# Performance work log

Measured on AMD Instinct MI355X. Metric: run time of the kernel, lower is better.

Reference implementation:

```python
import jax, jax.numpy as jnp
import numpy as np

B, S, V, E, H, L = 32, 512, 32000, 256, 512, 48


def setup_inputs() -> dict:
    key = jax.random.key(0)
    ks = jax.random.split(key, 12)
    tokens = jax.random.randint(ks[0], (B, S), 0, V)
    length = jax.random.randint(ks[1], (B,), S // 2, S + 1)
    labels = jax.random.randint(ks[2], (B, S), 0, L)
    embed_table = jax.random.normal(ks[3], (V, E), jnp.float32) * 0.1
    embed_table = embed_table.at[0].set(0.0)  # padding_idx = 0
    # torch LSTM gate order: i, f, g, o ; b = b_ih + b_hh folded together
    w_ih_f = jax.random.normal(ks[4], (4 * H, E), jnp.float32) * 0.05
    w_hh_f = jax.random.normal(ks[5], (4 * H, H), jnp.float32) * 0.05
    b_f = jnp.zeros((4 * H,), jnp.float32)
    w_ih_b = jax.random.normal(ks[6], (4 * H, E), jnp.float32) * 0.05
    w_hh_b = jax.random.normal(ks[7], (4 * H, H), jnp.float32) * 0.05
    b_b = jnp.zeros((4 * H,), jnp.float32)
    w_em = jax.random.normal(ks[8], (L, 2 * H), jnp.float32) * 0.02
    b_em = jnp.zeros((L,), jnp.float32)
    transition = jax.random.uniform(ks[9], (L, L), jnp.float32)  # torch.rand init
    return {"tokens": tokens, "length": length, "labels": labels,
            "embed_table": embed_table,
            "w_ih_f": w_ih_f, "w_hh_f": w_hh_f, "b_f": b_f,
            "w_ih_b": w_ih_b, "w_hh_b": w_hh_b, "b_b": b_b,
            "w_em": w_em, "b_em": b_em, "transition": transition}


def _lstm_dir(x, w_ih, w_hh, b, reverse):
    # x: [B,S,E] -> hidden states [B,S,H]
    xw = jnp.einsum('bse,ge->bsg', x, w_ih) + b  # precompute input projection [B,S,4H]
    if reverse:
        xw = xw[:, ::-1]
    Bn = x.shape[0]
    Hn = w_hh.shape[1]
    h0 = jnp.zeros((Bn, Hn), x.dtype)
    c0 = jnp.zeros((Bn, Hn), x.dtype)

    def step(carry, xt):
        h, c = carry
        gates = xt + h @ w_hh.T  # [B,4H]
        i, f, g, o = jnp.split(gates, 4, axis=-1)
        i = jax.nn.sigmoid(i)
        f = jax.nn.sigmoid(f)
        g = jnp.tanh(g)
        o = jax.nn.sigmoid(o)
        c = f * c + i * g
        h = o * jnp.tanh(c)
        return (h, c), h

    _, hs = jax.lax.scan(step, (h0, c0), jnp.swapaxes(xw, 0, 1))
    hs = jnp.swapaxes(hs, 0, 1)  # [B,S,H]
    if reverse:
        hs = hs[:, ::-1]
    return hs


def reference(tokens, length, labels, embed_table,
              w_ih_f, w_hh_f, b_f, w_ih_b, w_hh_b, b_b,
              w_em, b_em, transition):
    x = embed_table[tokens]                      # [B,S,E]
    hf = _lstm_dir(x, w_ih_f, w_hh_f, b_f, reverse=False)
    hb = _lstm_dir(x, w_ih_b, w_hh_b, b_b, reverse=True)
    h = jnp.concatenate([hf, hb], axis=-1)       # [B,S,2H]
    logits = jnp.einsum('bsh,lh->bsl', h, w_em) + b_em
    e = jnp.exp(logits)                          # emission = exp(linear), as in source
    T = jnp.exp(transition)                      # transition = exp(param), as in source
    Bn, Sn = tokens.shape
    pos = jnp.arange(Sn)[None, :]
    mask = pos < length[:, None]                 # [B,S] valid positions

    # gold path score: sum emissions over valid steps + transitions between them
    em_real = jnp.take_along_axis(e, labels[..., None], axis=-1)[..., 0]  # [B,S]
    real = jnp.sum(em_real * mask, axis=-1)
    trans_real = T[labels[:, :-1], labels[:, 1:]]                          # [B,S-1]
    real = real + jnp.sum(trans_real * mask[:, 1:], axis=-1)

    # forward algorithm, exactly as written in source:
    # alpha_new[k] = logsumexp_l( alpha[k] + T[k,l] + e_t[l] )
    alpha0 = e[:, 0, :]                          # [B,L]

    def step(alpha, inp):
        et, mt = inp                             # [B,L], [B]
        scores = alpha[:, :, None] + T[None, :, :] + et[:, None, :]  # [B,L,L]
        new = jax.nn.logsumexp(scores, axis=-1)
        alpha = jnp.where(mt[:, None], new, alpha)
        return alpha, None

    alpha, _ = jax.lax.scan(step, alpha0,
                            (jnp.swapaxes(e[:, 1:], 0, 1),
                             jnp.swapaxes(mask[:, 1:], 0, 1)))
    sum_score = jax.nn.logsumexp(alpha, axis=-1)  # [B]
    return sum_score - real                       # negative log probability per example
```

## Files before the change

### kernel.cpp

```cpp
#include <hip/hip_runtime.h>
#include <math.h>
#include <stdint.h>

#define Bn 32
#define Sn 512
#define En 256
#define Hn 512
#define Ln 48
#define G4 2048
#define NWG 32

typedef unsigned short u16;
typedef __attribute__((ext_vector_type(8))) __bf16 bf16x8;
typedef __attribute__((ext_vector_type(4))) float f32x4;

__device__ inline float bf2f(u16 u) {
    return __uint_as_float(((unsigned)u) << 16);
}
__device__ inline u16 f2bf(float f) {
    unsigned u = __float_as_uint(f);
    unsigned r = (u + 0x7fffu + ((u >> 16) & 1u)) >> 16;
    return (u16)r;
}
__device__ inline float sigmoidf_(float x) { return 1.f / (1.f + expf(-x)); }
__device__ inline float tanh_fast(float x) { return 2.f / (1.f + expf(-2.f * x)) - 1.f; }

__global__ __launch_bounds__(256) void prep_kernel(
    const int* __restrict__ tokens, const float* __restrict__ embed,
    const float* __restrict__ wihf, const float* __restrict__ wihb,
    const float* __restrict__ whhf, const float* __restrict__ whhb,
    const float* __restrict__ wem, const float* __restrict__ trans,
    u16* __restrict__ xbf, u16* __restrict__ wihf_b, u16* __restrict__ wihb_b,
    u16* __restrict__ whhf_b, u16* __restrict__ whhb_b, u16* __restrict__ wem_b,
    float* __restrict__ expT, float* __restrict__ alphaAcc,
    float* __restrict__ realAcc, unsigned* __restrict__ flags)
{
    size_t idx = (size_t)blockIdx.x * blockDim.x + threadIdx.x;
    size_t stride = (size_t)gridDim.x * blockDim.x;
    for (size_t i = idx; i < (size_t)Bn * Sn * En; i += stride) {
        size_t n = i >> 8; int ee = (int)(i & 255);
        int tok = tokens[n];
        xbf[i] = f2bf(embed[(size_t)tok * En + ee]);
    }
    for (size_t i = idx; i < (size_t)G4 * En; i += stride) {
        wihf_b[i] = f2bf(wihf[i]); wihb_b[i] = f2bf(wihb[i]);
    }
    for (size_t i = idx; i < (size_t)G4 * Hn; i += stride) {
        whhf_b[i] = f2bf(whhf[i]); whhb_b[i] = f2bf(whhb[i]);
    }
    for (size_t i = idx; i < (size_t)Ln * 2 * Hn; i += stride) wem_b[i] = f2bf(wem[i]);
    for (size_t i = idx; i < (size_t)Ln * Ln; i += stride) expT[i] = expf(trans[i]);
    for (size_t i = idx; i < (size_t)Bn * Ln; i += stride) alphaAcc[i] = 0.f;
    for (size_t i = idx; i < (size_t)Bn; i += stride) realAcc[i] = 0.f;
    for (size_t i = idx; i < (size_t)2 * Sn * NWG; i += stride) flags[i] = 0u;
}

__global__ __launch_bounds__(256) void gemm_xw(
    const u16* __restrict__ xbf, const u16* __restrict__ wihf_b,
    const u16* __restrict__ wihb_b, const float* __restrict__ bias_f,
    const float* __restrict__ bias_b, u16* __restrict__ xw_f, u16* __restrict__ xw_b)
{
    int mb = blockIdx.x, nb = blockIdx.y, dir = blockIdx.z;
    const u16* wih = dir ? wihb_b : wihf_b;
    const float* bias = dir ? bias_b : bias_f;
    u16* xw = dir ? xw_b : xw_f;

    __shared__ u16 At[64 * 136];
    __shared__ u16 Bt[64 * 136];

    int tid = threadIdx.x;
    int w = tid >> 6, lane = tid & 63;
    int lm = lane & 15, lkq = (lane >> 4) * 8;
    int Moff = (w & 1) * 32, Noff = (w >> 1) * 32;

    f32x4 zero = {0.f, 0.f, 0.f, 0.f};
    f32x4 acc[2][2] = {{zero, zero}, {zero, zero}};

    for (int kc = 0; kc < 2; kc++) {
        for (int c = tid; c < 1024; c += 256) {
            int r = c >> 4, cc = (c & 15) * 8;
            *(bf16x8*)&At[r * 136 + cc] =
                *(const bf16x8*)&xbf[((size_t)(mb * 64 + r)) * En + kc * 128 + cc];
            *(bf16x8*)&Bt[r * 136 + cc] =
                *(const bf16x8*)&wih[((size_t)(nb * 64 + r)) * En + kc * 128 + cc];
        }
        __syncthreads();
        #pragma unroll
        for (int ks = 0; ks < 4; ks++) {
            int k = ks * 32 + lkq;
            bf16x8 a0 = *(const bf16x8*)&At[(Moff + lm) * 136 + k];
            bf16x8 a1 = *(const bf16x8*)&At[(Moff + 16 + lm) * 136 + k];
            bf16x8 b0 = *(const bf16x8*)&Bt[(Noff + lm) * 136 + k];
            bf16x8 b1 = *(const bf16x8*)&Bt[(Noff + 16 + lm) * 136 + k];
            acc[0][0] = __builtin_amdgcn_mfma_f32_16x16x32_bf16(a0, b0, acc[0][0], 0, 0, 0);
            acc[0][1] = __builtin_amdgcn_mfma_f32_16x16x32_bf16(a0, b1, acc[0][1], 0, 0, 0);
            acc[1][0] = __builtin_amdgcn_mfma_f32_16x16x32_bf16(a1, b0, acc[1][0], 0, 0, 0);
            acc[1][1] = __builtin_amdgcn_mfma_f32_16x16x32_bf16(a1, b1, acc[1][1], 0, 0, 0);
        }
        __syncthreads();
    }
    #pragma unroll
    for (int mi = 0; mi < 2; mi++)
        #pragma unroll
        for (int ni = 0; ni < 2; ni++)
            #pragma unroll
            for (int reg = 0; reg < 4; reg++) {
                int row = Moff + mi * 16 + (lane >> 4) * 4 + reg;
                int col = Noff + ni * 16 + lm;
                int n = mb * 64 + row;
                int g = nb * 64 + col;
                int t = n & 511, b = n >> 9;
                float v = acc[mi][ni][reg] + bias[g];
                xw[((size_t)t * Bn + b) * G4 + g] = f2bf(v);
            }
}

__global__ __launch_bounds__(512) void lstm_rec(
    const u16* __restrict__ whhf_b, const u16* __restrict__ whhb_b,
    const u16* __restrict__ xw_f, const u16* __restrict__ xw_b,
    u16* __restrict__ hf, u16* __restrict__ hb, unsigned* __restrict__ flags)
{
    int wg = blockIdx.x;
    int dir = wg >> 5;
    int w = wg & 31;
    const u16* __restrict__ whh = dir ? whhb_b : whhf_b;
    const u16* __restrict__ xw  = dir ? xw_b  : xw_f;
    u16* __restrict__ hbuf = dir ? hb : hf;
    unsigned* flg = flags + (size_t)dir * Sn * NWG;

    __shared__ u16 Hs[32 * 512];
    __shared__ float Cp[4 * 32 * 17];
    __shared__ u16 hout[32 * 16];

    int tid = threadIdx.x;
    int wv = tid >> 6, lane = tid & 63;
    int lm = lane & 15, kq = lane >> 4;
    int mt = wv & 1, nt = wv >> 1;
    int b = tid >> 4, hc = tid & 15;

    bf16x8 Bf[16];
    {
        const u16* wrow = &whh[((size_t)nt * Hn + (size_t)w * 16 + lm) * Hn];
        #pragma unroll
        for (int ks = 0; ks < 16; ks++)
            Bf[ks] = *(const bf16x8*)&wrow[ks * 32 + kq * 8];
    }

    float c_state = 0.f;
    const f32x4 zero = {0.f, 0.f, 0.f, 0.f};

    for (int it = 0; it < Sn; it++) {
        int t = dir ? (Sn - 1 - it) : it;
        f32x4 acc = zero;

        if (it > 0) {
            int tprev = dir ? (t + 1) : (t - 1);
            if (tid < 64) {
                const unsigned* fp = flg + (size_t)(it - 1) * NWG + (tid & 31);
                int tries = 0;
                while (true) {
                    unsigned v;
                    asm volatile("global_load_dword %0, %1, off sc0 sc1\n\t"
                                 "s_waitcnt vmcnt(0)"
                                 : "=v"(v) : "v"(fp) : "memory");
                    if (__all(v != 0) || ++tries > 10000) break;
                    __builtin_amdgcn_s_sleep(1);
                }
            }
            __syncthreads();
            {
                const u16* base = &hbuf[((size_t)b * Sn + tprev) * Hn];
                const u16* p0 = base + (hc + 0) * 8;
                const u16* p1 = base + (hc + 16) * 8;
                const u16* p2 = base + (hc + 32) * 8;
                const u16* p3 = base + (hc + 48) * 8;
                f32x4 h0, h1, h2, h3;
                asm volatile(
                    "global_load_dwordx4 %0, %4, off sc0 sc1\n\t"
                    "global_load_dwordx4 %1, %5, off sc0 sc1\n\t"
                    "global_load_dwordx4 %2, %6, off sc0 sc1\n\t"
                    "global_load_dwordx4 %3, %7, off sc0 sc1\n\t"
                    "s_waitcnt vmcnt(0)"
                    : "=v"(h0), "=v"(h1), "=v"(h2), "=v"(h3)
                    : "v"(p0), "v"(p1), "v"(p2), "v"(p3)
                    : "memory");
                *(f32x4*)&Hs[(b * 64 + ((hc + 0) ^ (b & 7))) * 8] = h0;
                *(f32x4*)&Hs[(b * 64 + ((hc + 16) ^ (b & 7))) * 8] = h1;
                *(f32x4*)&Hs[(b * 64 + ((hc + 32) ^ (b & 7))) * 8] = h2;
                *(f32x4*)&Hs[(b * 64 + ((hc + 48) ^ (b & 7))) * 8] = h3;
            }
            __syncthreads();
            #pragma unroll
            for (int ks = 0; ks < 16; ks++) {
                bf16x8 a = *(const bf16x8*)
                    &Hs[((mt * 16 + lm) * 64 + ((ks * 4 + kq) ^ (lm & 7))) * 8];
                acc = __builtin_amdgcn_mfma_f32_16x16x32_bf16(a, Bf[ks], acc, 0, 0, 0);
            }
        }

        const u16* xp = &xw[((size_t)t * Bn + b) * G4 + (size_t)w * 16 + hc];
        float xg0 = bf2f(xp[0 * Hn]);
        float xg1 = bf2f(xp[1 * Hn]);
        float xg2 = bf2f(xp[2 * Hn]);
        float xg3 = bf2f(xp[3 * Hn]);

        #pragma unroll
        for (int reg = 0; reg < 4; reg++)
            Cp[(nt * 32 + mt * 16 + kq * 4 + reg) * 17 + lm] = acc[reg];
        __syncthreads();

        float g0 = Cp[(0 * 32 + b) * 17 + hc] + xg0;
        float g1 = Cp[(1 * 32 + b) * 17 + hc] + xg1;
        float g2 = Cp[(2 * 32 + b) * 17 + hc] + xg2;
        float g3 = Cp[(3 * 32 + b) * 17 + hc] + xg3;
        float i_ = sigmoidf_(g0);
        float f_ = sigmoidf_(g1);
        float gg = tanh_fast(g2);
        float o_ = sigmoidf_(g3);
        c_state = f_ * c_state + i_ * gg;
        float hv = o_ * tanh_fast(c_state);
        hout[tid] = f2bf(hv);
        __syncthreads();

        if (tid < 64) {
            int bq = lane >> 1, half = lane & 1;
            f32x4 hv8 = *(const f32x4*)&hout[lane * 8];
            u16* sp = &hbuf[((size_t)bq * Sn + t) * Hn + (size_t)w * 16 + half * 8];
            asm volatile("global_store_dwordx4 %0, %1, off sc0 sc1"
                         :: "v"(sp), "v"(hv8) : "memory");
            asm volatile("s_waitcnt vmcnt(0)" ::: "memory");
            if (tid == 0) {
                unsigned one = 1;
                unsigned* fq = flg + (size_t)it * NWG + w;
                asm volatile("global_store_dword %0, %1, off sc0 sc1\n\t"
                             "s_waitcnt vmcnt(0)"
                             :: "v"(fq), "v"(one) : "memory");
            }
        }
    }
}

__global__ __launch_bounds__(256) void emis(
    const u16* __restrict__ hf, const u16* __restrict__ hb,
    const u16* __restrict__ wem_b, const float* __restrict__ bem,
    float* __restrict__ e)
{
    int mb = blockIdx.x;
    int tid = threadIdx.x, wv = tid >> 6, lane = tid & 63;
    int lm = lane & 15, lkq = (lane >> 4) * 8;
    int row = mb * 64 + wv * 16;

    f32x4 zero = {0.f, 0.f, 0.f, 0.f};
    f32x4 acc[3] = {zero, zero, zero};
    for (int ks = 0; ks < 32; ks++) {
        int k = ks * 32 + lkq;
        const u16* hsrc = (ks < 16) ? &hf[(size_t)(row + lm) * Hn + k]
                                    : &hb[(size_t)(row + lm) * Hn + (k - 512)];
        bf16x8 a = *(const bf16x8*)hsrc;
        #pragma unroll
        for (int nt = 0; nt < 3; nt++) {
            bf16x8 bfr = *(const bf16x8*)&wem_b[(size_t)(nt * 16 + lm) * 1024 + k];
            acc[nt] = __builtin_amdgcn_mfma_f32_16x16x32_bf16(a, bfr, acc[nt], 0, 0, 0);
        }
    }
    #pragma unroll
    for (int nt = 0; nt < 3; nt++)
        #pragma unroll
        for (int reg = 0; reg < 4; reg++) {
            int r = row + (lane >> 4) * 4 + reg;
            int col = nt * 16 + lm;
            float lg = acc[nt][reg] + bem[col];
            e[(size_t)r * Ln + col] = expf(lg);
        }
}

__global__ __launch_bounds__(64) void crf_step(
    const float* __restrict__ e, const float* __restrict__ expT,
    const int* __restrict__ labels, const int* __restrict__ lengths,
    float* __restrict__ alphaAcc, float* __restrict__ realAcc)
{
    int bt = blockIdx.x;
    int b = bt >> 9, t = bt & 511;
    __shared__ float er[Ln];
    int tid = threadIdx.x;
    if (tid < Ln) er[tid] = e[(size_t)bt * Ln + tid];
    __syncthreads();
    bool inlen = t < lengths[b];
    if (t >= 1 && inlen && tid < Ln) {
        int i = tid;
        float m = -1e30f;
        for (int j = 0; j < Ln; j++) m = fmaxf(m, expT[i * Ln + j] + er[j]);
        float s = 0.f;
        for (int j = 0; j < Ln; j++) s += expf(expT[i * Ln + j] + er[j] - m);
        atomicAdd(&alphaAcc[b * Ln + i], m + logf(s));
    }
    if (tid == 0 && inlen) {
        int lab = labels[b * Sn + t];
        float r = er[lab];
        if (t >= 1) r += expT[labels[b * Sn + t - 1] * Ln + lab];
        atomicAdd(&realAcc[b], r);
    }
}

__global__ __launch_bounds__(64) void finalize(
    const float* __restrict__ e, const float* __restrict__ alphaAcc,
    const float* __restrict__ realAcc, float* __restrict__ out)
{
    int b = threadIdx.x;
    if (b >= Bn) return;
    float m = -1e30f;
    for (int i = 0; i < Ln; i++) {
        float a = e[((size_t)b * Sn) * Ln + i] + alphaAcc[b * Ln + i];
        m = fmaxf(m, a);
    }
    float s = 0.f;
    for (int i = 0; i < Ln; i++) {
        float a = e[((size_t)b * Sn) * Ln + i] + alphaAcc[b * Ln + i];
        s += expf(a - m);
    }
    out[b] = m + logf(s) - realAcc[b];
}

extern "C" void kernel_launch(void* const* d_in, const int* in_sizes, int n_in,
                              void* d_out, int out_size, void* d_ws, size_t ws_size,
                              hipStream_t stream)
{
    const int*   tokens = (const int*)d_in[0];
    const int*   length = (const int*)d_in[1];
    const int*   labels = (const int*)d_in[2];
    const float* embed  = (const float*)d_in[3];
    const float* wihf   = (const float*)d_in[4];
    const float* whhf   = (const float*)d_in[5];
    const float* bf     = (const float*)d_in[6];
    const float* wihb   = (const float*)d_in[7];
    const float* whhb   = (const float*)d_in[8];
    const float* bbv    = (const float*)d_in[9];
    const float* wem    = (const float*)d_in[10];
    const float* bem    = (const float*)d_in[11];
    const float* trans  = (const float*)d_in[12];
    float* out = (float*)d_out;

    char* p = (char*)d_ws;
    auto take = [&](size_t bytes) -> char* {
        char* q = p;
        p += (bytes + 255) & ~(size_t)255;
        return q;
    };
    u16* xw_f   = (u16*)take((size_t)Sn * Bn * G4 * 2);
    u16* xw_b   = (u16*)take((size_t)Sn * Bn * G4 * 2);
    u16* hf     = (u16*)take((size_t)Bn * Sn * Hn * 2);
    u16* hb     = (u16*)take((size_t)Bn * Sn * Hn * 2);
    u16* xbf    = (u16*)take((size_t)Bn * Sn * En * 2);
    u16* wihf_b = (u16*)take((size_t)G4 * En * 2);
    u16* wihb_b = (u16*)take((size_t)G4 * En * 2);
    u16* whhf_b = (u16*)take((size_t)G4 * Hn * 2);
    u16* whhb_b = (u16*)take((size_t)G4 * Hn * 2);
    u16* wem_b  = (u16*)take((size_t)Ln * 2 * Hn * 2);
    float* e        = (float*)take((size_t)Bn * Sn * Ln * 4);
    float* expT     = (float*)take((size_t)Ln * Ln * 4);
    float* alphaAcc = (float*)take((size_t)Bn * Ln * 4);
    float* realAcc  = (float*)take((size_t)Bn * 4);
    unsigned* flags = (unsigned*)take((size_t)2 * Sn * NWG * 4);
    if ((size_t)(p - (char*)d_ws) > ws_size) return;

    prep_kernel<<<4096, 256, 0, stream>>>(tokens, embed, wihf, wihb, whhf, whhb, wem, trans,
                                          xbf, wihf_b, wihb_b, whhf_b, whhb_b, wem_b,
                                          expT, alphaAcc, realAcc, flags);

    dim3 g1(256, 32, 2);
    gemm_xw<<<g1, 256, 0, stream>>>(xbf, wihf_b, wihb_b, bf, bbv, xw_f, xw_b);

    void* ra[] = { (void*)&whhf_b, (void*)&whhb_b, (void*)&xw_f, (void*)&xw_b,
                   (void*)&hf, (void*)&hb, (void*)&flags };
    hipLaunchCooperativeKernel((const void*)lstm_rec, dim3(2 * NWG), dim3(512), ra, 0, stream);

    emis<<<256, 256, 0, stream>>>(hf, hb, wem_b, bem, e);
    crf_step<<<Bn * Sn, 64, 0, stream>>>(e, expT, labels, length, alphaAcc, realAcc);
    finalize<<<1, 64, 0, stream>>>(e, alphaAcc, realAcc, out);
}
```

Baseline: 2.135 ms.

## Replace per-step flag handshake with sentinel-poisoned hidden-state polling

Removes the per-timestep flag array in the cooperative LSTM recurrence. Instead, the hidden-state buffers are pre-filled with a bf16 sentinel pattern, and each thread spins directly on its own h loads until none of the values equals the sentinel. This drops the flag store, its waitcnt, and the separate poll-then-barrier round trip from every step. The xw gate loads are also hoisted ahead of the wait. The cost is a larger init pass over both h buffers, plus reliance on the sentinel (a bf16 NaN) never being produced as a real h value and on 16-byte stores being seen atomically.

Result: faster. 1.920 ms (-10.1%).

```diff
diff --git a/kernel.cpp b/kernel.cpp
--- a/kernel.cpp
+++ b/kernel.cpp
@@ -9,6 +9,7 @@
 #define Ln 48
 #define G4 2048
 #define NWG 32
+#define SENT16 0x7FFFu
 
 typedef unsigned short u16;
 typedef __attribute__((ext_vector_type(8))) __bf16 bf16x8;
@@ -24,6 +25,17 @@
 }
 __device__ inline float sigmoidf_(float x) { return 1.f / (1.f + expf(-x)); }
 __device__ inline float tanh_fast(float x) { return 2.f / (1.f + expf(-2.f * x)) - 1.f; }
+
+__device__ inline int chunkBad(f32x4 v) {
+    unsigned x0 = __float_as_uint(v.x), x1 = __float_as_uint(v.y);
+    unsigned x2 = __float_as_uint(v.z), x3 = __float_as_uint(v.w);
+    int bad = 0;
+    bad |= ((x0 & 0xFFFFu) == SENT16) | ((x0 >> 16) == SENT16);
+    bad |= ((x1 & 0xFFFFu) == SENT16) | ((x1 >> 16) == SENT16);
+    bad |= ((x2 & 0xFFFFu) == SENT16) | ((x2 >> 16) == SENT16);
+    bad |= ((x3 & 0xFFFFu) == SENT16) | ((x3 >> 16) == SENT16);
+    return bad;
+}
 
 __global__ __launch_bounds__(256) void prep_kernel(
     const int* __restrict__ tokens, const float* __restrict__ embed,
@@ -33,7 +45,8 @@
     u16* __restrict__ xbf, u16* __restrict__ wihf_b, u16* __restrict__ wihb_b,
     u16* __restrict__ whhf_b, u16* __restrict__ whhb_b, u16* __restrict__ wem_b,
     float* __restrict__ expT, float* __restrict__ alphaAcc,
-    float* __restrict__ realAcc, unsigned* __restrict__ flags)
+    float* __restrict__ realAcc, unsigned* __restrict__ hf32,
+    unsigned* __restrict__ hb32)
 {
     size_t idx = (size_t)blockIdx.x * blockDim.x + threadIdx.x;
     size_t stride = (size_t)gridDim.x * blockDim.x;
@@ -52,7 +65,10 @@
     for (size_t i = idx; i < (size_t)Ln * Ln; i += stride) expT[i] = expf(trans[i]);
     for (size_t i = idx; i < (size_t)Bn * Ln; i += stride) alphaAcc[i] = 0.f;
     for (size_t i = idx; i < (size_t)Bn; i += stride) realAcc[i] = 0.f;
-    for (size_t i = idx; i < (size_t)2 * Sn * NWG; i += stride) flags[i] = 0u;
+    const unsigned sp = (SENT16 << 16) | SENT16;
+    for (size_t i = idx; i < (size_t)Bn * Sn * Hn / 2; i += stride) {
+        hf32[i] = sp; hb32[i] = sp;
+    }
 }
 
 __global__ __launch_bounds__(256) void gemm_xw(
@@ -118,7 +134,7 @@
 __global__ __launch_bounds__(512) void lstm_rec(
     const u16* __restrict__ whhf_b, const u16* __restrict__ whhb_b,
     const u16* __restrict__ xw_f, const u16* __restrict__ xw_b,
-    u16* __restrict__ hf, u16* __restrict__ hb, unsigned* __restrict__ flags)
+    u16* __restrict__ hf, u16* __restrict__ hb)
 {
     int wg = blockIdx.x;
     int dir = wg >> 5;
@@ -126,7 +142,6 @@
     const u16* __restrict__ whh = dir ? whhb_b : whhf_b;
     const u16* __restrict__ xw  = dir ? xw_b  : xw_f;
     u16* __restrict__ hbuf = dir ? hb : hf;
-    unsigned* flg = flags + (size_t)dir * Sn * NWG;
 
     __shared__ u16 Hs[32 * 512];
     __shared__ float Cp[4 * 32 * 17];
@@ -153,28 +168,22 @@
         int t = dir ? (Sn - 1 - it) : it;
         f32x4 acc = zero;
 
+        const u16* xp = &xw[((size_t)t * Bn + b) * G4 + (size_t)w * 16 + hc];
+        float xg0 = bf2f(xp[0 * Hn]);
+        float xg1 = bf2f(xp[1 * Hn]);
+        float xg2 = bf2f(xp[2 * Hn]);
+        float xg3 = bf2f(xp[3 * Hn]);
+
         if (it > 0) {
             int tprev = dir ? (t + 1) : (t - 1);
-            if (tid < 64) {
-                const unsigned* fp = flg + (size_t)(it - 1) * NWG + (tid & 31);
-                int tries = 0;
-                while (true) {
-                    unsigned v;
-                    asm volatile("global_load_dword %0, %1, off sc0 sc1\n\t"
-                                 "s_waitcnt vmcnt(0)"
-                                 : "=v"(v) : "v"(fp) : "memory");
-                    if (__all(v != 0) || ++tries > 10000) break;
-                    __builtin_amdgcn_s_sleep(1);
-                }
-            }
-            __syncthreads();
-            {
-                const u16* base = &hbuf[((size_t)b * Sn + tprev) * Hn];
-                const u16* p0 = base + (hc + 0) * 8;
-                const u16* p1 = base + (hc + 16) * 8;
-                const u16* p2 = base + (hc + 32) * 8;
-                const u16* p3 = base + (hc + 48) * 8;
-                f32x4 h0, h1, h2, h3;
+            const u16* base = &hbuf[((size_t)b * Sn + tprev) * Hn];
+            const u16* p0 = base + (hc + 0) * 8;
+            const u16* p1 = base + (hc + 16) * 8;
+            const u16* p2 = base + (hc + 32) * 8;
+            const u16* p3 = base + (hc + 48) * 8;
+            f32x4 h0, h1, h2, h3;
+            int tries = 0;
+            while (true) {
                 asm volatile(
                     "global_load_dwordx4 %0, %4, off sc0 sc1\n\t"
                     "global_load_dwordx4 %1, %5, off sc0 sc1\n\t"
@@ -184,11 +193,13 @@
                     : "=v"(h0), "=v"(h1), "=v"(h2), "=v"(h3)
                     : "v"(p0), "v"(p1), "v"(p2), "v"(p3)
                     : "memory");
-                *(f32x4*)&Hs[(b * 64 + ((hc + 0) ^ (b & 7))) * 8] = h0;
-                *(f32x4*)&Hs[(b * 64 + ((hc + 16) ^ (b & 7))) * 8] = h1;
-                *(f32x4*)&Hs[(b * 64 + ((hc + 32) ^ (b & 7))) * 8] = h2;
-                *(f32x4*)&Hs[(b * 64 + ((hc + 48) ^ (b & 7))) * 8] = h3;
+                if (!(chunkBad(h0) | chunkBad(h1) | chunkBad(h2) | chunkBad(h3))) break;
+                if (++tries > 65536) break;
             }
+            *(f32x4*)&Hs[(b * 64 + ((hc + 0) ^ (b & 7))) * 8] = h0;
+            *(f32x4*)&Hs[(b * 64 + ((hc + 16) ^ (b & 7))) * 8] = h1;
+            *(f32x4*)&Hs[(b * 64 + ((hc + 32) ^ (b & 7))) * 8] = h2;
+            *(f32x4*)&Hs[(b * 64 + ((hc + 48) ^ (b & 7))) * 8] = h3;
             __syncthreads();
             #pragma unroll
             for (int ks = 0; ks < 16; ks++) {
@@ -197,12 +208,6 @@
                 acc = __builtin_amdgcn_mfma_f32_16x16x32_bf16(a, Bf[ks], acc, 0, 0, 0);
             }
         }
-
-        const u16* xp = &xw[((size_t)t * Bn + b) * G4 + (size_t)w * 16 + hc];
-        float xg0 = bf2f(xp[0 * Hn]);
-        float xg1 = bf2f(xp[1 * Hn]);
-        float xg2 = bf2f(xp[2 * Hn]);
-        float xg3 = bf2f(xp[3 * Hn]);
 
         #pragma unroll
         for (int reg = 0; reg < 4; reg++)
@@ -228,14 +233,6 @@
             u16* sp = &hbuf[((size_t)bq * Sn + t) * Hn + (size_t)w * 16 + half * 8];
             asm volatile("global_store_dwordx4 %0, %1, off sc0 sc1"
                          :: "v"(sp), "v"(hv8) : "memory");
-            asm volatile("s_waitcnt vmcnt(0)" ::: "memory");
-            if (tid == 0) {
-                unsigned one = 1;
-                unsigned* fq = flg + (size_t)it * NWG + w;
-                asm volatile("global_store_dword %0, %1, off sc0 sc1\n\t"
-                             "s_waitcnt vmcnt(0)"
-                             :: "v"(fq), "v"(one) : "memory");
-            }
         }
     }
 }
@@ -360,18 +357,18 @@
     float* expT     = (float*)take((size_t)Ln * Ln * 4);
     float* alphaAcc = (float*)take((size_t)Bn * Ln * 4);
     float* realAcc  = (float*)take((size_t)Bn * 4);
-    unsigned* flags = (unsigned*)take((size_t)2 * Sn * NWG * 4);
     if ((size_t)(p - (char*)d_ws) > ws_size) return;
 
     prep_kernel<<<4096, 256, 0, stream>>>(tokens, embed, wihf, wihb, whhf, whhb, wem, trans,
                                           xbf, wihf_b, wihb_b, whhf_b, whhb_b, wem_b,
-                                          expT, alphaAcc, realAcc, flags);
+                                          expT, alphaAcc, realAcc,
+                                          (unsigned*)hf, (unsigned*)hb);
 
     dim3 g1(256, 32, 2);
     gemm_xw<<<g1, 256, 0, stream>>>(xbf, wihf_b, wihb_b, bf, bbv, xw_f, xw_b);
 
     void* ra[] = { (void*)&whhf_b, (void*)&whhb_b, (void*)&xw_f, (void*)&xw_b,
-                   (void*)&hf, (void*)&hb, (void*)&flags };
+                   (void*)&hf, (void*)&hb };
     hipLaunchCooperativeKernel((const void*)lstm_rec, dim3(2 * NWG), dim3(512), ra, 0, stream);
 
     emis<<<256, 256, 0, stream>>>(hf, hb, wem_b, bem, e);
```

## Add sentinel-validated hidden-state loads and relax flag ordering in LSTM recurrence

Applied to the files above, without the earlier changes.

Fills the hidden-state buffers with a bf16 sentinel (0x7FFF) in prep and re-polls the h loads until no sentinel lane is seen. This allows the vmcnt wait between the h store and the flag store to be removed, so the flag may become visible before the data. Also drops the s_sleep in the flag spin, hoists the xw gate loads ahead of the wait, and splits the MFMA chain into two accumulators. The cost is a large extra memset in prep and a correctness dependence on no real bf16 value matching the sentinel.

After: 1.987 ms. 6.9% less time.

```diff
diff --git a/kernel.cpp b/kernel.cpp
--- a/kernel.cpp
+++ b/kernel.cpp
@@ -9,6 +9,7 @@
 #define Ln 48
 #define G4 2048
 #define NWG 32
+#define SENT16 0x7FFFu
 
 typedef unsigned short u16;
 typedef __attribute__((ext_vector_type(8))) __bf16 bf16x8;
@@ -24,6 +25,17 @@
 }
 __device__ inline float sigmoidf_(float x) { return 1.f / (1.f + expf(-x)); }
 __device__ inline float tanh_fast(float x) { return 2.f / (1.f + expf(-2.f * x)) - 1.f; }
+
+__device__ inline unsigned badMask(f32x4 v) {
+    unsigned acc = 0;
+    #pragma unroll
+    for (int i = 0; i < 4; i++) {
+        unsigned d = __float_as_uint(v[i]);
+        unsigned x = d ^ 0x7FFF7FFFu;
+        acc |= (x - 0x00010001u) & ~x & 0x80008000u;
+    }
+    return acc;
+}
 
 __global__ __launch_bounds__(256) void prep_kernel(
     const int* __restrict__ tokens, const float* __restrict__ embed,
@@ -33,7 +45,8 @@
     u16* __restrict__ xbf, u16* __restrict__ wihf_b, u16* __restrict__ wihb_b,
     u16* __restrict__ whhf_b, u16* __restrict__ whhb_b, u16* __restrict__ wem_b,
     float* __restrict__ expT, float* __restrict__ alphaAcc,
-    float* __restrict__ realAcc, unsigned* __restrict__ flags)
+    float* __restrict__ realAcc, unsigned* __restrict__ hf32,
+    unsigned* __restrict__ hb32, unsigned* __restrict__ flags)
 {
     size_t idx = (size_t)blockIdx.x * blockDim.x + threadIdx.x;
     size_t stride = (size_t)gridDim.x * blockDim.x;
@@ -52,6 +65,10 @@
     for (size_t i = idx; i < (size_t)Ln * Ln; i += stride) expT[i] = expf(trans[i]);
     for (size_t i = idx; i < (size_t)Bn * Ln; i += stride) alphaAcc[i] = 0.f;
     for (size_t i = idx; i < (size_t)Bn; i += stride) realAcc[i] = 0.f;
+    const unsigned sp = (SENT16 << 16) | SENT16;
+    for (size_t i = idx; i < (size_t)Bn * Sn * Hn / 2; i += stride) {
+        hf32[i] = sp; hb32[i] = sp;
+    }
     for (size_t i = idx; i < (size_t)2 * Sn * NWG; i += stride) flags[i] = 0u;
 }
 
@@ -153,28 +170,36 @@
         int t = dir ? (Sn - 1 - it) : it;
         f32x4 acc = zero;
 
+        const u16* xp = &xw[((size_t)t * Bn + b) * G4 + (size_t)w * 16 + hc];
+        float xg0 = bf2f(xp[0 * Hn]);
+        float xg1 = bf2f(xp[1 * Hn]);
+        float xg2 = bf2f(xp[2 * Hn]);
+        float xg3 = bf2f(xp[3 * Hn]);
+
         if (it > 0) {
             int tprev = dir ? (t + 1) : (t - 1);
+
             if (tid < 64) {
-                const unsigned* fp = flg + (size_t)(it - 1) * NWG + (tid & 31);
+                const unsigned* fp = flg + (size_t)(it - 1) * NWG + (lane & 31);
                 int tries = 0;
                 while (true) {
                     unsigned v;
                     asm volatile("global_load_dword %0, %1, off sc0 sc1\n\t"
                                  "s_waitcnt vmcnt(0)"
                                  : "=v"(v) : "v"(fp) : "memory");
-                    if (__all(v != 0) || ++tries > 10000) break;
-                    __builtin_amdgcn_s_sleep(1);
+                    if (__all(v != 0) || ++tries > (1 << 16)) break;
                 }
             }
             __syncthreads();
-            {
-                const u16* base = &hbuf[((size_t)b * Sn + tprev) * Hn];
-                const u16* p0 = base + (hc + 0) * 8;
-                const u16* p1 = base + (hc + 16) * 8;
-                const u16* p2 = base + (hc + 32) * 8;
-                const u16* p3 = base + (hc + 48) * 8;
-                f32x4 h0, h1, h2, h3;
+
+            const u16* base = &hbuf[((size_t)b * Sn + tprev) * Hn];
+            const u16* p0 = base + (hc + 0) * 8;
+            const u16* p1 = base + (hc + 16) * 8;
+            const u16* p2 = base + (hc + 32) * 8;
+            const u16* p3 = base + (hc + 48) * 8;
+            f32x4 h0, h1, h2, h3;
+            int tries = 0;
+            while (true) {
                 asm volatile(
                     "global_load_dwordx4 %0, %4, off sc0 sc1\n\t"
                     "global_load_dwordx4 %1, %5, off sc0 sc1\n\t"
@@ -184,25 +209,27 @@
                     : "=v"(h0), "=v"(h1), "=v"(h2), "=v"(h3)
                     : "v"(p0), "v"(p1), "v"(p2), "v"(p3)
                     : "memory");
-                *(f32x4*)&Hs[(b * 64 + ((hc + 0) ^ (b & 7))) * 8] = h0;
-                *(f32x4*)&Hs[(b * 64 + ((hc + 16) ^ (b & 7))) * 8] = h1;
-                *(f32x4*)&Hs[(b * 64 + ((hc + 32) ^ (b & 7))) * 8] = h2;
-                *(f32x4*)&Hs[(b * 64 + ((hc + 48) ^ (b & 7))) * 8] = h3;
+                if (!(badMask(h0) | badMask(h1) | badMask(h2) | badMask(h3))) break;
+                if (++tries > (1 << 16)) break;
             }
+            *(f32x4*)&Hs[(b * 64 + ((hc + 0) ^ (b & 7))) * 8] = h0;
+            *(f32x4*)&Hs[(b * 64 + ((hc + 16) ^ (b & 7))) * 8] = h1;
+            *(f32x4*)&Hs[(b * 64 + ((hc + 32) ^ (b & 7))) * 8] = h2;
+            *(f32x4*)&Hs[(b * 64 + ((hc + 48) ^ (b & 7))) * 8] = h3;
             __syncthreads();
+
+            f32x4 aa = zero, ab = zero;
             #pragma unroll
-            for (int ks = 0; ks < 16; ks++) {
-                bf16x8 a = *(const bf16x8*)
-                    &Hs[((mt * 16 + lm) * 64 + ((ks * 4 + kq) ^ (lm & 7))) * 8];
-                acc = __builtin_amdgcn_mfma_f32_16x16x32_bf16(a, Bf[ks], acc, 0, 0, 0);
+            for (int ks2 = 0; ks2 < 8; ks2++) {
+                bf16x8 a0 = *(const bf16x8*)
+                    &Hs[((mt * 16 + lm) * 64 + (((2 * ks2) * 4 + kq) ^ (lm & 7))) * 8];
+                aa = __builtin_amdgcn_mfma_f32_16x16x32_bf16(a0, Bf[2 * ks2], aa, 0, 0, 0);
+                bf16x8 a1 = *(const bf16x8*)
+                    &Hs[((mt * 16 + lm) * 64 + (((2 * ks2 + 1) * 4 + kq) ^ (lm & 7))) * 8];
+                ab = __builtin_amdgcn_mfma_f32_16x16x32_bf16(a1, Bf[2 * ks2 + 1], ab, 0, 0, 0);
             }
-        }
-
-        const u16* xp = &xw[((size_t)t * Bn + b) * G4 + (size_t)w * 16 + hc];
-        float xg0 = bf2f(xp[0 * Hn]);
-        float xg1 = bf2f(xp[1 * Hn]);
-        float xg2 = bf2f(xp[2 * Hn]);
-        float xg3 = bf2f(xp[3 * Hn]);
+            acc = aa + ab;
+        }
 
         #pragma unroll
         for (int reg = 0; reg < 4; reg++)
@@ -228,12 +255,10 @@
             u16* sp = &hbuf[((size_t)bq * Sn + t) * Hn + (size_t)w * 16 + half * 8];
             asm volatile("global_store_dwordx4 %0, %1, off sc0 sc1"
                          :: "v"(sp), "v"(hv8) : "memory");
-            asm volatile("s_waitcnt vmcnt(0)" ::: "memory");
-            if (tid == 0) {
+            if (lane == 0) {
                 unsigned one = 1;
                 unsigned* fq = flg + (size_t)it * NWG + w;
-                asm volatile("global_store_dword %0, %1, off sc0 sc1\n\t"
-                             "s_waitcnt vmcnt(0)"
+                asm volatile("global_store_dword %0, %1, off sc0 sc1"
                              :: "v"(fq), "v"(one) : "memory");
             }
         }
@@ -365,7 +390,8 @@
 
     prep_kernel<<<4096, 256, 0, stream>>>(tokens, embed, wihf, wihb, whhf, whhb, wem, trans,
                                           xbf, wihf_b, wihb_b, whhf_b, whhb_b, wem_b,
-                                          expT, alphaAcc, realAcc, flags);
+                                          expT, alphaAcc, realAcc,
+                                          (unsigned*)hf, (unsigned*)hb, flags);
 
     dim3 g1(256, 32, 2);
     gemm_xw<<<g1, 256, 0, stream>>>(xbf, wihf_b, wihb_b, bf, bbv, xw_f, xw_b);
```
